# Kernel tuning notes

Hardware: AMD Instinct MI355X
Metric: run time of the kernel (lower is better)

Reference implementation:

```python
import jax, jax.numpy as jnp
import numpy as np

N, C, T1, H, W = 8, 256, 16, 28, 28
T2, V = 64, 25
REL = min(C, C) // 8  # 32


def setup_inputs() -> dict:
    key = jax.random.key(0)
    ks = jax.random.split(key, 10)
    s = 0.02
    return {
        "image": jax.random.normal(ks[0], (N, C, T1, H, W), jnp.float32),
        "motion": jax.random.normal(ks[1], (N, C, T2, V), jnp.float32),
        # 1x1 conv weights stored as [out, in]
        "w_mq": jax.random.normal(ks[2], (REL, C), jnp.float32) * s,   # motion_query Conv2d
        "b_mq": jax.random.normal(ks[3], (REL,), jnp.float32) * s,
        "w_iq": jax.random.normal(ks[4], (REL, C), jnp.float32) * s,   # img_query Conv3d
        "b_iq": jax.random.normal(ks[5], (REL,), jnp.float32) * s,
        "w_iv": jax.random.normal(ks[6], (C, C), jnp.float32) * s,     # img_value Conv3d
        "b_iv": jax.random.normal(ks[7], (C,), jnp.float32) * s,
        "w_att": jax.random.normal(ks[8], (C, REL), jnp.float32) * s,  # att Conv2d
        "b_att": jax.random.normal(ks[9], (C,), jnp.float32) * s,
    }


def reference(image, motion, w_mq, b_mq, w_iq, b_iq, w_iv, b_iv, w_att, b_att):
    n, c, t1, h, w = image.shape
    _, c2, t2, v = motion.shape

    # Q: 1x1x1 conv then mean over H*W. Conv is pointwise-linear so it commutes
    # exactly with the spatial mean (bias is spatially constant) -> mean first.
    img_mean = image.mean(axis=(-2, -1))                       # [N, C, T1]
    Q = jnp.einsum('nct,rc->nrt', img_mean, w_iq) + b_iq[None, :, None]  # [N, REL, T1]

    # K: 1x1 conv on motion then adaptive_avg_pool2d to (T1, 1).
    # pooling commutes with the pointwise conv -> pool first.
    mot_pool = motion.reshape(n, c2, t1, t2 // t1, v).mean(axis=(3, 4))  # [N, C2, T1]
    K = jnp.einsum('nct,rc->nrt', mot_pool, w_mq) + b_mq[None, :, None]  # [N, REL, T1]

    # V: 1x1x1 conv on image, flattened spatial.
    Vv = jnp.einsum('ncthw,dc->ndthw', image, w_iv) + b_iv[None, :, None, None, None]
    Vv = Vv.reshape(n, c, t1, h * w)                           # [N, C, T1, HW]

    # scores[n,r,i,j] = tanh(K[n,r,i] - Q[n,r,j])
    scores = jnp.tanh(K[:, :, :, None] - Q[:, :, None, :])     # [N, REL, T1, T1]

    # att conv (REL->C, 1x1), scale, add identity
    att = jnp.einsum('nrij,cr->ncij', scores, w_att) + b_att[None, :, None, None]
    att = att / t1 + jnp.eye(t1, dtype=att.dtype)[None, None]  # [N, C, T1, T1]

    y = jnp.einsum('ncij,ncjv->nciv', att, Vv)                 # [N, C, T1, HW]
    return y.reshape(n, c, t1, h, w)
```

## Files before the change

### kernel.cpp

```cpp
#include <hip/hip_runtime.h>
#include <hip/hip_bf16.h>

typedef __bf16 bf16_t;
typedef bf16_t bf16x8 __attribute__((ext_vector_type(8)));
typedef float  f32x4  __attribute__((ext_vector_type(4)));

#define NN  8
#define CC  256
#define T1C 16
#define HWC 784
#define T2C 64
#define VC  25
#define RELC 32

__global__ void k_cvt_w(const float* __restrict__ w, bf16_t* __restrict__ wb) {
    int i = (blockIdx.x * 256 + threadIdx.x) * 4;
    float4 v = *(const float4*)(w + i);
    union { bf16_t b[4]; uint2 u; } o;
    o.b[0] = (__bf16)v.x; o.b[1] = (__bf16)v.y;
    o.b[2] = (__bf16)v.z; o.b[3] = (__bf16)v.w;
    *(uint2*)(wb + i) = o.u;
}

__global__ void k_mot(const float* __restrict__ mot, float* __restrict__ pool) {
    int bc = blockIdx.x;
    const float* src = mot + (long)bc * (T2C * VC);
    __shared__ float s[T2C * VC];
    for (int i = threadIdx.x; i < T2C * VC; i += 64) s[i] = src[i];
    __syncthreads();
    if (threadIdx.x < 16) {
        float a = 0.f;
        const float* p = s + threadIdx.x * 100;
        #pragma unroll 4
        for (int k = 0; k < 100; k++) a += p[k];
        pool[bc * 16 + threadIdx.x] = a * (1.0f / 100.0f);
    }
}

__global__ void k_transpose(const float* __restrict__ img, bf16_t* __restrict__ imT,
                            float* __restrict__ mean_raw, int n0) {
    int hwb = blockIdx.x, cb = blockIdx.y;
    int z = blockIdx.z; int nl = z >> 4, j = z & 15; int n = n0 + nl;
    int hw0 = hwb * 56, c0 = cb * 64;
    __shared__ __align__(16) bf16_t tile[56][68];
    __shared__ float ssum[64];
    int t = threadIdx.x;
    if (t < 64) ssum[t] = 0.f;
    __syncthreads();
    for (int fl = t; fl < 896; fl += 256) {
        int cl = fl / 14, f4 = fl % 14;
        float4 v = *(const float4*)(img + (((long)n * CC + c0 + cl) * T1C + j) * HWC + hw0 + f4 * 4);
        int hwl = f4 * 4;
        tile[hwl + 0][cl] = (__bf16)v.x;
        tile[hwl + 1][cl] = (__bf16)v.y;
        tile[hwl + 2][cl] = (__bf16)v.z;
        tile[hwl + 3][cl] = (__bf16)v.w;
        atomicAdd(&ssum[cl], v.x + v.y + v.z + v.w);
    }
    __syncthreads();
    if (t < 64) atomicAdd(mean_raw + ((long)n * CC + c0 + t) * T1C + j, ssum[t]);
    for (int fl = t; fl < 896; fl += 256) {
        int hwl = fl / 16, cg = fl % 16;
        ushort4 o = *(ushort4*)(&tile[hwl][cg * 4]);
        *(ushort4*)(imT + ((((long)nl * T1C + j) * HWC + hw0 + hwl) * CC + c0 + cg * 4)) = o;
    }
}

__global__ void k_att(const float* __restrict__ mean_raw, const float* __restrict__ pool,
                      const float* __restrict__ w_mq, const float* __restrict__ b_mq,
                      const float* __restrict__ w_iq, const float* __restrict__ b_iq,
                      const float* __restrict__ w_att, const float* __restrict__ b_att,
                      float* __restrict__ att_t, int n0) {
    int n = n0 + blockIdx.x;
    __shared__ float Qs[RELC * T1C], Ks[RELC * T1C], sc[RELC * T1C * T1C];
    int t = threadIdx.x;
    for (int o = t; o < 2 * RELC * T1C; o += 256) {
        int which = (o >= RELC * T1C);
        int rt = which ? o - RELC * T1C : o;
        int r = rt >> 4, tt = rt & 15;
        const float* wrow = which ? (w_mq + r * CC) : (w_iq + r * CC);
        const float* src  = which ? (pool + (long)n * CC * T1C + tt)
                                  : (mean_raw + (long)n * CC * T1C + tt);
        float scl = which ? 1.0f : (1.0f / 784.0f);
        float a = 0.f;
        for (int c = 0; c < CC; c++) a += wrow[c] * src[c * T1C];
        a = a * scl + (which ? b_mq[r] : b_iq[r]);
        (which ? Ks : Qs)[rt] = a;
    }
    __syncthreads();
    for (int o = t; o < RELC * T1C * T1C; o += 256) {
        int r = o >> 8, i = (o >> 4) & 15, j = o & 15;
        sc[o] = tanhf(Ks[r * 16 + i] - Qs[r * 16 + j]);
    }
    __syncthreads();
    int c = t;
    float wr[RELC];
    #pragma unroll
    for (int r = 0; r < RELC; r++) wr[r] = w_att[c * RELC + r];
    float bc = b_att[c];
    float* outp = att_t + ((long)n * CC + c) * 256;
    for (int j = 0; j < 16; j++) {
        for (int i = 0; i < 16; i++) {
            float a = bc;
            #pragma unroll
            for (int r = 0; r < RELC; r++) a += wr[r] * sc[r * 256 + i * 16 + j];
            a = a * (1.0f / 16.0f) + (i == j ? 1.0f : 0.0f);
            outp[j * 16 + i] = a;
        }
    }
}

__launch_bounds__(256, 2)
__global__ void k_main(const bf16_t* __restrict__ imT, const bf16_t* __restrict__ wb,
                       const float* __restrict__ att_t, const float* __restrict__ b_iv,
                       float* __restrict__ out, int n0) {
    const int COLS = 128, PITCH = 136, KHALF = 128;
    __shared__ __align__(16) bf16_t Bl[COLS * PITCH];
    int t = threadIdx.x;
    int h = blockIdx.x;
    int nl = blockIdx.y; int n = n0 + nl;
    int hw0 = h * 8;
    int lane = t & 63, wave = t >> 6;
    int l15 = lane & 15, quad = lane >> 4;

    f32x4 acc[4][8];
    f32x4 zf = {0.f, 0.f, 0.f, 0.f};
    #pragma unroll
    for (int mt = 0; mt < 4; mt++)
        #pragma unroll
        for (int nt = 0; nt < 8; nt++) acc[mt][nt] = zf;

    const bf16_t* imTn = imT + (long)nl * T1C * HWC * CC;

    for (int kst = 0; kst < 2; ++kst) {
        __syncthreads();
        for (int s = t; s < 2048; s += 256) {
            int col = s >> 4, cc = s & 15;
            int j = col >> 3, hwl = col & 7;
            uint4 v = *(const uint4*)(imTn + ((long)j * HWC + hw0 + hwl) * CC + kst * KHALF + cc * 8);
            *(uint4*)(&Bl[col * PITCH + cc * 8]) = v;
        }
        __syncthreads();
        #pragma unroll
        for (int ks = 0; ks < 4; ++ks) {
            int ko = ks * 32 + quad * 8;
            bf16x8 a[4];
            #pragma unroll
            for (int mt = 0; mt < 4; ++mt)
                a[mt] = *(const bf16x8*)(wb + ((long)(wave * 64 + mt * 16 + l15)) * CC + kst * KHALF + ko);
            #pragma unroll
            for (int nt = 0; nt < 8; ++nt) {
                bf16x8 b = *(const bf16x8*)(&Bl[(nt * 16 + l15) * PITCH + ko]);
                #pragma unroll
                for (int mt = 0; mt < 4; ++mt)
                    acc[mt][nt] = __builtin_amdgcn_mfma_f32_16x16x32_bf16(a[mt], b, acc[mt][nt], 0, 0, 0);
            }
        }
    }
    __syncthreads();

    float* Vbase = ((float*)Bl) + wave * (16 * 132);
    const float* attn = att_t + (long)n * CC * 256;
    for (int mt = 0; mt < 4; ++mt) {
        #pragma unroll
        for (int nt = 0; nt < 8; ++nt) {
            #pragma unroll
            for (int r = 0; r < 4; r++) {
                int crow = quad * 4 + r;
                float biv = b_iv[wave * 64 + mt * 16 + crow];
                Vbase[crow * 132 + nt * 16 + l15] = acc[mt][nt][r] + biv;
            }
        }
        __syncthreads();
        int cg = wave * 64 + mt * 16 + l15;
        const float* Vrow = Vbase + l15 * 132;
        const float* arow = attn + (long)cg * 256 + quad * 4;
        f32x4 y0[4], y1[4];
        #pragma unroll
        for (int ii = 0; ii < 4; ii++) { y0[ii] = zf; y1[ii] = zf; }
        #pragma unroll
        for (int j = 0; j < 16; j++) {
            f32x4 v0 = *(const f32x4*)(Vrow + j * 8);
            f32x4 v1 = *(const f32x4*)(Vrow + j * 8 + 4);
            f32x4 aa = *(const f32x4*)(arow + j * 16);
            #pragma unroll
            for (int ii = 0; ii < 4; ii++) {
                y0[ii] += aa[ii] * v0;
                y1[ii] += aa[ii] * v1;
            }
        }
        float* ob = out + ((long)n * CC + cg) * T1C * HWC + hw0;
        #pragma unroll
        for (int ii = 0; ii < 4; ii++) {
            int i = quad * 4 + ii;
            *(f32x4*)(ob + (long)i * HWC)     = y0[ii];
            *(f32x4*)(ob + (long)i * HWC + 4) = y1[ii];
        }
        __syncthreads();
    }
}

extern "C" void kernel_launch(void* const* d_in, const int* in_sizes, int n_in,
                              void* d_out, int out_size, void* d_ws, size_t ws_size,
                              hipStream_t stream) {
    const float* image = (const float*)d_in[0];
    const float* motion = (const float*)d_in[1];
    const float* w_mq = (const float*)d_in[2];
    const float* b_mq = (const float*)d_in[3];
    const float* w_iq = (const float*)d_in[4];
    const float* b_iq = (const float*)d_in[5];
    const float* w_iv = (const float*)d_in[6];
    const float* b_iv = (const float*)d_in[7];
    const float* w_att = (const float*)d_in[8];
    const float* b_att = (const float*)d_in[9];
    float* out = (float*)d_out;

    const size_t IMT_PER_N = (size_t)T1C * HWC * CC * 2;
    const size_t W_BYTES = (size_t)CC * CC * 2;
    const size_t MEAN_BYTES = (size_t)NN * CC * T1C * 4;
    const size_t ATT_BYTES = (size_t)NN * CC * 256 * 4;
    size_t fixed = W_BYTES + MEAN_BYTES * 2 + ATT_BYTES;

    int chunkN = 8;
    while (chunkN > 1 && (size_t)chunkN * IMT_PER_N + fixed > ws_size) chunkN >>= 1;

    char* p = (char*)d_ws;
    bf16_t* imT = (bf16_t*)p;  p += (size_t)chunkN * IMT_PER_N;
    bf16_t* wbf = (bf16_t*)p;  p += W_BYTES;
    float* mean = (float*)p;   p += MEAN_BYTES;
    float* pool = (float*)p;   p += MEAN_BYTES;
    float* att  = (float*)p;

    hipMemsetAsync(mean, 0, MEAN_BYTES, stream);
    k_cvt_w<<<64, 256, 0, stream>>>(w_iv, wbf);
    k_mot<<<NN * CC, 64, 0, stream>>>(motion, pool);

    for (int n0 = 0; n0 < NN; n0 += chunkN) {
        k_transpose<<<dim3(14, 4, chunkN * 16), 256, 0, stream>>>(image, imT, mean, n0);
        k_att<<<chunkN, 256, 0, stream>>>(mean, pool, w_mq, b_mq, w_iq, b_iq,
                                          w_att, b_att, att, n0);
        k_main<<<dim3(98, chunkN), 256, 0, stream>>>(imT, wbf, att, b_iv, out, n0);
    }
}
```

Before: 411.9 us.

## Split attention kernel for parallelism, shuffle-reduce channel sums, drop epilogue barriers

The single-block-per-sample attention kernel is split into two kernels. k_qk builds Q/K from transposed shared-memory copies of mean and pool and writes tanh scores to a workspace. k_att2 runs 16 channel-group blocks per sample and writes att rows with coalesced stores. In the transpose kernel, per-channel sums now use wave shuffles and direct global atomics instead of LDS atomics plus an extra barrier. The __syncthreads in k_main's epilogue are removed because each wave only touches its own LDS region. The cost is one extra launch and a small scores buffer in the workspace.

```diff
diff --git a/kernel.cpp b/kernel.cpp
--- a/kernel.cpp
+++ b/kernel.cpp
@@ -43,70 +43,111 @@
     int z = blockIdx.z; int nl = z >> 4, j = z & 15; int n = n0 + nl;
     int hw0 = hwb * 56, c0 = cb * 64;
     __shared__ __align__(16) bf16_t tile[56][68];
-    __shared__ float ssum[64];
-    int t = threadIdx.x;
-    if (t < 64) ssum[t] = 0.f;
+    int t = threadIdx.x;
+    int f4 = t & 15, cl0 = t >> 4;
+    float psum[4];
+    #pragma unroll
+    for (int k = 0; k < 4; k++) {
+        int cl = cl0 + 16 * k;
+        float4 v = {0.f, 0.f, 0.f, 0.f};
+        if (f4 < 14)
+            v = *(const float4*)(img + (((long)n * CC + c0 + cl) * T1C + j) * HWC + hw0 + f4 * 4);
+        psum[k] = v.x + v.y + v.z + v.w;
+        if (f4 < 14) {
+            int hwl = f4 * 4;
+            tile[hwl + 0][cl] = (__bf16)v.x;
+            tile[hwl + 1][cl] = (__bf16)v.y;
+            tile[hwl + 2][cl] = (__bf16)v.z;
+            tile[hwl + 3][cl] = (__bf16)v.w;
+        }
+    }
+    #pragma unroll
+    for (int k = 0; k < 4; k++) {
+        float s = psum[k];
+        s += __shfl_xor(s, 1); s += __shfl_xor(s, 2);
+        s += __shfl_xor(s, 4); s += __shfl_xor(s, 8);
+        psum[k] = s;
+    }
+    if (f4 == 0) {
+        #pragma unroll
+        for (int k = 0; k < 4; k++)
+            atomicAdd(mean_raw + ((long)n * CC + c0 + cl0 + 16 * k) * T1C + j, psum[k]);
+    }
     __syncthreads();
     for (int fl = t; fl < 896; fl += 256) {
-        int cl = fl / 14, f4 = fl % 14;
-        float4 v = *(const float4*)(img + (((long)n * CC + c0 + cl) * T1C + j) * HWC + hw0 + f4 * 4);
-        int hwl = f4 * 4;
-        tile[hwl + 0][cl] = (__bf16)v.x;
-        tile[hwl + 1][cl] = (__bf16)v.y;
-        tile[hwl + 2][cl] = (__bf16)v.z;
-        tile[hwl + 3][cl] = (__bf16)v.w;
-        atomicAdd(&ssum[cl], v.x + v.y + v.z + v.w);
-    }
-    __syncthreads();
-    if (t < 64) atomicAdd(mean_raw + ((long)n * CC + c0 + t) * T1C + j, ssum[t]);
-    for (int fl = t; fl < 896; fl += 256) {
-        int hwl = fl / 16, cg = fl % 16;
+        int hwl = fl >> 4, cg = fl & 15;
         ushort4 o = *(ushort4*)(&tile[hwl][cg * 4]);
         *(ushort4*)(imT + ((((long)nl * T1C + j) * HWC + hw0 + hwl) * CC + c0 + cg * 4)) = o;
     }
 }
 
-__global__ void k_att(const float* __restrict__ mean_raw, const float* __restrict__ pool,
-                      const float* __restrict__ w_mq, const float* __restrict__ b_mq,
-                      const float* __restrict__ w_iq, const float* __restrict__ b_iq,
-                      const float* __restrict__ w_att, const float* __restrict__ b_att,
-                      float* __restrict__ att_t, int n0) {
+__global__ void k_qk(const float* __restrict__ mean_raw, const float* __restrict__ pool,
+                     const float* __restrict__ w_mq, const float* __restrict__ b_mq,
+                     const float* __restrict__ w_iq, const float* __restrict__ b_iq,
+                     float* __restrict__ scoresG, int n0) {
     int n = n0 + blockIdx.x;
-    __shared__ float Qs[RELC * T1C], Ks[RELC * T1C], sc[RELC * T1C * T1C];
-    int t = threadIdx.x;
-    for (int o = t; o < 2 * RELC * T1C; o += 256) {
-        int which = (o >= RELC * T1C);
-        int rt = which ? o - RELC * T1C : o;
+    const int PQ = 260;
+    __shared__ float meanT[16 * PQ];
+    __shared__ float poolT[16 * PQ];
+    __shared__ float Qs[512], Ks[512];
+    int t = threadIdx.x;
+    {
+        const float* mr = mean_raw + ((long)n * CC + t) * 16;
+        const float* pr = pool + ((long)n * CC + t) * 16;
+        #pragma unroll
+        for (int tt = 0; tt < 16; tt++) {
+            meanT[tt * PQ + t] = mr[tt] * (1.0f / 784.0f);
+            poolT[tt * PQ + t] = pr[tt];
+        }
+    }
+    __syncthreads();
+    for (int item = t; item < 1024; item += 256) {
+        int which = item >> 9;
+        int rt = item & 511;
         int r = rt >> 4, tt = rt & 15;
         const float* wrow = which ? (w_mq + r * CC) : (w_iq + r * CC);
-        const float* src  = which ? (pool + (long)n * CC * T1C + tt)
-                                  : (mean_raw + (long)n * CC * T1C + tt);
-        float scl = which ? 1.0f : (1.0f / 784.0f);
+        const float* src = (which ? poolT : meanT) + tt * PQ;
         float a = 0.f;
-        for (int c = 0; c < CC; c++) a += wrow[c] * src[c * T1C];
-        a = a * scl + (which ? b_mq[r] : b_iq[r]);
+        #pragma unroll 8
+        for (int c = 0; c < CC; c++) a += wrow[c] * src[c];
+        a += which ? b_mq[r] : b_iq[r];
         (which ? Ks : Qs)[rt] = a;
     }
     __syncthreads();
-    for (int o = t; o < RELC * T1C * T1C; o += 256) {
-        int r = o >> 8, i = (o >> 4) & 15, j = o & 15;
-        sc[o] = tanhf(Ks[r * 16 + i] - Qs[r * 16 + j]);
-    }
-    __syncthreads();
-    int c = t;
+    float* sg = scoresG + (long)n * 8192;
+    for (int o = t; o < 8192; o += 256) {
+        int r = o >> 8, jj = (o >> 4) & 15, ii = o & 15;
+        sg[o] = tanhf(Ks[r * 16 + ii] - Qs[r * 16 + jj]);
+    }
+}
+
+__global__ void k_att2(const float* __restrict__ scoresG, const float* __restrict__ w_att,
+                       const float* __restrict__ b_att, float* __restrict__ att_t, int n0) {
+    int n = n0 + blockIdx.x;
+    int cb = blockIdx.y;
+    __shared__ float sc[8192];
+    __shared__ float wa[16][33];
+    int t = threadIdx.x;
+    const float* sg = scoresG + (long)n * 8192;
+    for (int o = t; o < 8192; o += 256) sc[o] = sg[o];
+    for (int o = t; o < 512; o += 256) {
+        int cl = o >> 5, r = o & 31;
+        wa[cl][r] = w_att[(cb * 16 + cl) * RELC + r];
+    }
+    __syncthreads();
+    int cl = t >> 4, ii = t & 15;
+    int c = cb * 16 + cl;
+    float bc = b_att[c];
     float wr[RELC];
     #pragma unroll
-    for (int r = 0; r < RELC; r++) wr[r] = w_att[c * RELC + r];
-    float bc = b_att[c];
+    for (int r = 0; r < RELC; r++) wr[r] = wa[cl][r];
     float* outp = att_t + ((long)n * CC + c) * 256;
+    #pragma unroll
     for (int j = 0; j < 16; j++) {
-        for (int i = 0; i < 16; i++) {
-            float a = bc;
-            #pragma unroll
-            for (int r = 0; r < RELC; r++) a += wr[r] * sc[r * 256 + i * 16 + j];
-            a = a * (1.0f / 16.0f) + (i == j ? 1.0f : 0.0f);
-            outp[j * 16 + i] = a;
-        }
+        float a = bc;
+        #pragma unroll
+        for (int r = 0; r < RELC; r++) a += wr[r] * sc[r * 256 + j * 16 + ii];
+        outp[j * 16 + ii] = a * (1.0f / 16.0f) + (ii == j ? 1.0f : 0.0f);
     }
 }
 
@@ -114,8 +155,8 @@
 __global__ void k_main(const bf16_t* __restrict__ imT, const bf16_t* __restrict__ wb,
                        const float* __restrict__ att_t, const float* __restrict__ b_iv,
                        float* __restrict__ out, int n0) {
-    const int COLS = 128, PITCH = 136, KHALF = 128;
-    __shared__ __align__(16) bf16_t Bl[COLS * PITCH];
+    const int PITCH = 136, KHALF = 128;
+    __shared__ __align__(16) bf16_t Bl[128 * PITCH];
     int t = threadIdx.x;
     int h = blockIdx.x;
     int nl = blockIdx.y; int n = n0 + nl;
@@ -171,7 +212,6 @@
                 Vbase[crow * 132 + nt * 16 + l15] = acc[mt][nt][r] + biv;
             }
         }
-        __syncthreads();
         int cg = wave * 64 + mt * 16 + l15;
         const float* Vrow = Vbase + l15 * 132;
         const float* arow = attn + (long)cg * 256 + quad * 4;
@@ -196,7 +236,6 @@
             *(f32x4*)(ob + (long)i * HWC)     = y0[ii];
             *(f32x4*)(ob + (long)i * HWC + 4) = y1[ii];
         }
-        __syncthreads();
     }
 }
 
@@ -219,7 +258,8 @@
     const size_t W_BYTES = (size_t)CC * CC * 2;
     const size_t MEAN_BYTES = (size_t)NN * CC * T1C * 4;
     const size_t ATT_BYTES = (size_t)NN * CC * 256 * 4;
-    size_t fixed = W_BYTES + MEAN_BYTES * 2 + ATT_BYTES;
+    const size_t SC_BYTES = (size_t)NN * 8192 * 4;
+    size_t fixed = W_BYTES + MEAN_BYTES * 2 + ATT_BYTES + SC_BYTES;
 
     int chunkN = 8;
     while (chunkN > 1 && (size_t)chunkN * IMT_PER_N + fixed > ws_size) chunkN >>= 1;
@@ -229,7 +269,8 @@
     bf16_t* wbf = (bf16_t*)p;  p += W_BYTES;
     float* mean = (float*)p;   p += MEAN_BYTES;
     float* pool = (float*)p;   p += MEAN_BYTES;
-    float* att  = (float*)p;
+    float* att  = (float*)p;   p += ATT_BYTES;
+    float* scoresG = (float*)p;
 
     hipMemsetAsync(mean, 0, MEAN_BYTES, stream);
     k_cvt_w<<<64, 256, 0, stream>>>(w_iv, wbf);
@@ -237,8 +278,8 @@
 
     for (int n0 = 0; n0 < NN; n0 += chunkN) {
         k_transpose<<<dim3(14, 4, chunkN * 16), 256, 0, stream>>>(image, imT, mean, n0);
-        k_att<<<chunkN, 256, 0, stream>>>(mean, pool, w_mq, b_mq, w_iq, b_iq,
-                                          w_att, b_att, att, n0);
+        k_qk<<<chunkN, 256, 0, stream>>>(mean, pool, w_mq, b_mq, w_iq, b_iq, scoresG, n0);
+        k_att2<<<dim3(chunkN, 16), 256, 0, stream>>>(scoresG, w_att, b_att, att, n0);
         k_main<<<dim3(98, chunkN), 256, 0, stream>>>(imT, wbf, att, b_iv, out, n0);
     }
 }
```

Measured after the change: 380.1 us. 1.08x faster.
